# Performance work log

Hardware: AMD Instinct MI355X
Metric: run time of the kernel (lower is better)

The kernel has to match this reference:

```python
import jax, jax.numpy as jnp
import numpy as np

B, S, H = 64, 4096, 512

def setup_inputs() -> dict:
    key = jax.random.key(0)
    ks = jax.random.split(key, 8)
    decoder_output = jax.random.normal(ks[0], (B, H), dtype=jnp.float32)
    encoder_output = jax.random.normal(ks[1], (B, S, 2 * H), dtype=jnp.float32)
    mask = jax.random.randint(ks[2], (B, S), 0, 2).astype(bool)
    mask = mask.at[:, 0].set(True)  # guarantee at least one valid position per row
    sc_h = 1.0 / np.sqrt(2 * H)
    sc_s = 1.0 / np.sqrt(H)
    W_h_w = jax.random.uniform(ks[3], (H, 2 * H), jnp.float32, -sc_h, sc_h)
    W_h_b = jax.random.uniform(ks[4], (H,), jnp.float32, -sc_h, sc_h)
    W_s_w = jax.random.uniform(ks[5], (H, H), jnp.float32, -sc_s, sc_s)
    W_s_b = jax.random.uniform(ks[6], (H,), jnp.float32, -sc_s, sc_s)
    v_w = jax.random.uniform(ks[7], (1, H), jnp.float32, -sc_s, sc_s)
    return {"decoder_output": decoder_output, "encoder_output": encoder_output,
            "mask": mask, "W_h_w": W_h_w, "W_h_b": W_h_b,
            "W_s_w": W_s_w, "W_s_b": W_s_b, "v_w": v_w}

def reference(decoder_output, encoder_output, mask, W_h_w, W_h_b, W_s_w, W_s_b, v_w):
    # enc proj: [B,S,H]; dec proj: [B,H] broadcast over S
    enc = jnp.einsum('bse,he->bsh', encoder_output, W_h_w) + W_h_b
    dec = decoder_output @ W_s_w.T + W_s_b  # [B,H]
    x = jnp.tanh(enc + dec[:, None, :])     # [B,S,H]
    scores = jnp.einsum('bsh,h->bs', x, v_w[0])  # [B,S]
    masked = jnp.where(mask, scores, -jnp.inf)
    return jax.nn.softmax(masked, axis=-1)
```

## Files before the change

### kernel.cpp

```cpp
#include <hip/hip_runtime.h>
#include <math.h>

typedef __attribute__((ext_vector_type(8))) short bf16x8;
typedef __attribute__((ext_vector_type(4))) float f32x4;
typedef __attribute__((ext_vector_type(4))) unsigned short u16x4;

#define NB 64
#define NS 4096
#define NH 512
#define NE 1024
#define APITCH 80

__device__ __forceinline__ unsigned short f2bf(float f) {
  unsigned int u = __float_as_uint(f);
  u += 0x7fffu + ((u >> 16) & 1u);
  return (unsigned short)(u >> 16);
}

__device__ __forceinline__ float fast_tanh(float x) {
  float e = __expf(2.0f * x);
  return 1.0f - 2.0f * __builtin_amdgcn_rcpf(e + 1.0f);
}

__global__ __launch_bounds__(256) void prep_b_kernel(const float* __restrict__ W,
                                                     unsigned short* __restrict__ Bp) {
  const int t = blockIdx.x * 256 + threadIdx.x;
  const int lane = t & 63;
  const int ni = (t >> 6) & 3;
  const int kb = (t >> 8) & 31;
  const int w = t >> 13;
  const int col = w * 64 + ni * 16 + (lane & 15);
  const int k0 = kb * 32 + (lane >> 4) * 8;
  const float* src = W + col * NE + k0;
  float4 a = *(const float4*)src;
  float4 b = *(const float4*)(src + 4);
  union { bf16x8 v; unsigned short u[8]; } p;
  p.u[0] = f2bf(a.x); p.u[1] = f2bf(a.y); p.u[2] = f2bf(a.z); p.u[3] = f2bf(a.w);
  p.u[4] = f2bf(b.x); p.u[5] = f2bf(b.y); p.u[6] = f2bf(b.z); p.u[7] = f2bf(b.w);
  *(bf16x8*)(Bp + (long long)t * 8) = p.v;
}

__global__ __launch_bounds__(512) void prep_dec_kernel(const float* __restrict__ dec,
                                                       const float* __restrict__ Wsw,
                                                       const float* __restrict__ Wsb,
                                                       const float* __restrict__ Whb,
                                                       float* __restrict__ decb) {
  int b = blockIdx.x;
  int h = threadIdx.x;
  const float4* dr = (const float4*)(dec + b * NH);
  const float4* wr = (const float4*)(Wsw + h * NH);
  float sum = Wsb[h] + Whb[h];
#pragma unroll 8
  for (int i = 0; i < NH / 4; ++i) {
    float4 a = dr[i], w = wr[i];
    sum += a.x * w.x + a.y * w.y + a.z * w.z + a.w * w.w;
  }
  decb[b * NH + h] = sum;
}

__global__ __launch_bounds__(512, 4) void fused_main(const float* __restrict__ enc,
                                                     const unsigned short* __restrict__ Bp,
                                                     const float* __restrict__ decb,
                                                     const float* __restrict__ vw,
                                                     float* __restrict__ scores) {
  __shared__ __align__(16) char As[2][64 * APITCH];
  __shared__ float ssc[64];

  const int tid = threadIdx.x;
  const int lane = tid & 63;
  const int wave = tid >> 6;
  const int r15 = lane & 15;
  const int c4 = lane >> 4;
  const long long m0 = (long long)blockIdx.x * 64;

  if (tid < 64) ssc[tid] = 0.0f;

  const int arow = tid >> 3;
  const int achk = tid & 7;
  const float* aload = enc + (m0 + arow) * NE + achk * 4;
  const int awr = arow * APITCH + achk * 8;
  const int rdb = r15 * APITCH + c4 * 16;

  const unsigned short* const bb = Bp + (long long)wave * 32 * 2048 + lane * 8;

  f32x4 acc[4][4];
#pragma unroll
  for (int mi = 0; mi < 4; ++mi)
#pragma unroll
    for (int ni = 0; ni < 4; ++ni) {
      f32x4 z = {0.f, 0.f, 0.f, 0.f};
      acc[mi][ni] = z;
    }

  bf16x8 bEv[4], bOd[4];
#pragma unroll
  for (int ni = 0; ni < 4; ++ni) bEv[ni] = *(const bf16x8*)(bb + ni * 512);
  {
    float4 a0 = *(const float4*)(aload);
    unsigned int w0, w1;
    asm("v_cvt_pk_bf16_f32 %0, %1, %2" : "=v"(w0) : "v"(a0.x), "v"(a0.y));
    asm("v_cvt_pk_bf16_f32 %0, %1, %2" : "=v"(w1) : "v"(a0.z), "v"(a0.w));
    uint2 wv; wv.x = w0; wv.y = w1;
    *(uint2*)(&As[0][0] + awr) = wv;
  }
  asm volatile("s_waitcnt lgkmcnt(0)" ::: "memory");
  __builtin_amdgcn_s_barrier();

#pragma unroll
  for (int t = 0; t < 32; ++t) {
    float4 aT;
    if (t < 31) {
      aT = *(const float4*)(aload + (t + 1) * 32);
      const bf16x8* bp = (const bf16x8*)(bb + (t + 1) * 2048);
      if (t & 1) {
#pragma unroll
        for (int ni = 0; ni < 4; ++ni) bEv[ni] = bp[ni * 64];
      } else {
#pragma unroll
        for (int ni = 0; ni < 4; ++ni) bOd[ni] = bp[ni * 64];
      }
    }
    const char* Ab = &As[t & 1][0];
    bf16x8 af0 = *(const bf16x8*)(Ab + rdb);
    bf16x8 af1 = *(const bf16x8*)(Ab + 16 * APITCH + rdb);
    bf16x8 af2 = *(const bf16x8*)(Ab + 32 * APITCH + rdb);
    bf16x8 af3 = *(const bf16x8*)(Ab + 48 * APITCH + rdb);
    __builtin_amdgcn_sched_barrier(0);
    __builtin_amdgcn_s_setprio(1);
#pragma unroll
    for (int ni = 0; ni < 4; ++ni)
      acc[0][ni] = __builtin_amdgcn_mfma_f32_16x16x32_bf16(
          af0, (t & 1) ? bOd[ni] : bEv[ni], acc[0][ni], 0, 0, 0);
#pragma unroll
    for (int ni = 0; ni < 4; ++ni)
      acc[1][ni] = __builtin_amdgcn_mfma_f32_16x16x32_bf16(
          af1, (t & 1) ? bOd[ni] : bEv[ni], acc[1][ni], 0, 0, 0);
#pragma unroll
    for (int ni = 0; ni < 4; ++ni)
      acc[2][ni] = __builtin_amdgcn_mfma_f32_16x16x32_bf16(
          af2, (t & 1) ? bOd[ni] : bEv[ni], acc[2][ni], 0, 0, 0);
#pragma unroll
    for (int ni = 0; ni < 4; ++ni)
      acc[3][ni] = __builtin_amdgcn_mfma_f32_16x16x32_bf16(
          af3, (t & 1) ? bOd[ni] : bEv[ni], acc[3][ni], 0, 0, 0);
    __builtin_amdgcn_s_setprio(0);
    if (t < 31) {
      unsigned int w0, w1;
      asm("v_cvt_pk_bf16_f32 %0, %1, %2" : "=v"(w0) : "v"(aT.x), "v"(aT.y));
      asm("v_cvt_pk_bf16_f32 %0, %1, %2" : "=v"(w1) : "v"(aT.z), "v"(aT.w));
      uint2 wv; wv.x = w0; wv.y = w1;
      *(uint2*)(&As[(t + 1) & 1][0] + awr) = wv;
    }
    asm volatile("s_waitcnt lgkmcnt(0)" ::: "memory");
    __builtin_amdgcn_sched_barrier(0);
    __builtin_amdgcn_s_barrier();
  }

  const int bidx = (int)(m0 >> 12);
  const float* decrow = decb + bidx * NH;
  float part[4][4];
#pragma unroll
  for (int mi = 0; mi < 4; ++mi)
#pragma unroll
    for (int j = 0; j < 4; ++j) part[mi][j] = 0.f;

#pragma unroll
  for (int ni = 0; ni < 4; ++ni) {
    int col = (wave << 6) + ni * 16 + r15;
    float vc = vw[col];
    float dc = decrow[col];
#pragma unroll
    for (int mi = 0; mi < 4; ++mi)
#pragma unroll
      for (int j = 0; j < 4; ++j)
        part[mi][j] += vc * fast_tanh(acc[mi][ni][j] + dc);
  }
#pragma unroll
  for (int off = 1; off < 16; off <<= 1)
#pragma unroll
    for (int mi = 0; mi < 4; ++mi)
#pragma unroll
      for (int j = 0; j < 4; ++j)
        part[mi][j] += __shfl_xor(part[mi][j], off, 64);

  if (r15 == 0) {
#pragma unroll
    for (int mi = 0; mi < 4; ++mi)
#pragma unroll
      for (int j = 0; j < 4; ++j)
        atomicAdd(&ssc[mi * 16 + c4 * 4 + j], part[mi][j]);
  }
  __syncthreads();
  if (tid < 64) scores[m0 + tid] = ssc[tid];
}

__global__ __launch_bounds__(1024) void softmax_kernel(const float* __restrict__ scores,
                                                       const int* __restrict__ mask,
                                                       float* __restrict__ out) {
  __shared__ float rmax[16];
  __shared__ float rsum[16];
  const int b = blockIdx.x;
  const int t = threadIdx.x;
  const int wid = t >> 6;
  const int ln = t & 63;
  const int base = b * NS;

  float s[4];
  int mk[4];
  float mx = -INFINITY;
#pragma unroll
  for (int i = 0; i < 4; ++i) {
    int idx = t + i * 1024;
    s[i] = scores[base + idx];
    mk[i] = mask[base + idx];
    if (mk[i]) mx = fmaxf(mx, s[i]);
  }
#pragma unroll
  for (int off = 1; off < 64; off <<= 1) mx = fmaxf(mx, __shfl_xor(mx, off, 64));
  if (ln == 0) rmax[wid] = mx;
  __syncthreads();
  float m2 = -INFINITY;
#pragma unroll
  for (int i = 0; i < 16; ++i) m2 = fmaxf(m2, rmax[i]);

  float e[4];
  float sum = 0.f;
#pragma unroll
  for (int i = 0; i < 4; ++i) {
    e[i] = mk[i] ? expf(s[i] - m2) : 0.f;
    sum += e[i];
  }
#pragma unroll
  for (int off = 1; off < 64; off <<= 1) sum += __shfl_xor(sum, off, 64);
  if (ln == 0) rsum[wid] = sum;
  __syncthreads();
  float tot = 0.f;
#pragma unroll
  for (int i = 0; i < 16; ++i) tot += rsum[i];
  float inv = 1.0f / tot;
#pragma unroll
  for (int i = 0; i < 4; ++i) {
    int idx = t + i * 1024;
    out[base + idx] = e[i] * inv;
  }
}

extern "C" void kernel_launch(void* const* d_in, const int* in_sizes, int n_in,
                              void* d_out, int out_size, void* d_ws, size_t ws_size,
                              hipStream_t stream) {
  const float* dec = (const float*)d_in[0];
  const float* enc = (const float*)d_in[1];
  const int* mask = (const int*)d_in[2];
  const float* Whw = (const float*)d_in[3];
  const float* Whb = (const float*)d_in[4];
  const float* Wsw = (const float*)d_in[5];
  const float* Wsb = (const float*)d_in[6];
  const float* vw = (const float*)d_in[7];
  float* out = (float*)d_out;

  unsigned short* Bp = (unsigned short*)d_ws;
  float* decb = (float*)((char*)d_ws + (1 << 20));
  float* scoresb = (float*)((char*)d_ws + (1 << 20) + (128 << 10));

  prep_b_kernel<<<dim3(256), dim3(256), 0, stream>>>(Whw, Bp);
  prep_dec_kernel<<<dim3(64), dim3(512), 0, stream>>>(dec, Wsw, Wsb, Whb, decb);
  fused_main<<<dim3(4096), dim3(512), 0, stream>>>(enc, Bp, decb, vw, scoresb);
  softmax_kernel<<<dim3(64), dim3(1024), 0, stream>>>(scoresb, mask, out);
}
```

Baseline: 435.7 us.

## Double M tile to 128 rows with 4-stage LDS ring and fragment prefetch

Each block now covers 128 encoder rows instead of 64, so every W_h fragment read from global memory feeds twice as many MFMAs, halving B-operand traffic per output. The A tile is staged through a 4-deep LDS ring with global loads issued two steps ahead, and A fragments for the next step are read from LDS between MFMAs. The cost is twice the accumulator registers and LDS per block, with occupancy lowered to 2 blocks per CU, which may reduce latency hiding.

```diff
diff --git a/kernel.cpp b/kernel.cpp
--- a/kernel.cpp
+++ b/kernel.cpp
@@ -58,34 +58,34 @@
   decb[b * NH + h] = sum;
 }
 
-__global__ __launch_bounds__(512, 4) void fused_main(const float* __restrict__ enc,
+__global__ __launch_bounds__(512, 2) void fused_main(const float* __restrict__ enc,
                                                      const unsigned short* __restrict__ Bp,
                                                      const float* __restrict__ decb,
                                                      const float* __restrict__ vw,
                                                      float* __restrict__ scores) {
-  __shared__ __align__(16) char As[2][64 * APITCH];
-  __shared__ float ssc[64];
+  __shared__ __align__(16) char As[4][128 * APITCH];
+  __shared__ float ssc[128];
 
   const int tid = threadIdx.x;
   const int lane = tid & 63;
   const int wave = tid >> 6;
   const int r15 = lane & 15;
   const int c4 = lane >> 4;
-  const long long m0 = (long long)blockIdx.x * 64;
-
-  if (tid < 64) ssc[tid] = 0.0f;
-
-  const int arow = tid >> 3;
-  const int achk = tid & 7;
-  const float* aload = enc + (m0 + arow) * NE + achk * 4;
-  const int awr = arow * APITCH + achk * 8;
+  const long long m0 = (long long)blockIdx.x * 128;
+
+  if (tid < 128) ssc[tid] = 0.0f;
+
+  const int arow = tid >> 2;
+  const int achk = tid & 3;
+  const float* aload = enc + (m0 + arow) * NE + achk * 8;
+  const int awr = arow * APITCH + achk * 16;
   const int rdb = r15 * APITCH + c4 * 16;
 
   const unsigned short* const bb = Bp + (long long)wave * 32 * 2048 + lane * 8;
 
-  f32x4 acc[4][4];
-#pragma unroll
-  for (int mi = 0; mi < 4; ++mi)
+  f32x4 acc[8][4];
+#pragma unroll
+  for (int mi = 0; mi < 8; ++mi)
 #pragma unroll
     for (int ni = 0; ni < 4; ++ni) {
       f32x4 z = {0.f, 0.f, 0.f, 0.f};
@@ -95,22 +95,30 @@
   bf16x8 bEv[4], bOd[4];
 #pragma unroll
   for (int ni = 0; ni < 4; ++ni) bEv[ni] = *(const bf16x8*)(bb + ni * 512);
-  {
-    float4 a0 = *(const float4*)(aload);
-    unsigned int w0, w1;
-    asm("v_cvt_pk_bf16_f32 %0, %1, %2" : "=v"(w0) : "v"(a0.x), "v"(a0.y));
-    asm("v_cvt_pk_bf16_f32 %0, %1, %2" : "=v"(w1) : "v"(a0.z), "v"(a0.w));
-    uint2 wv; wv.x = w0; wv.y = w1;
-    *(uint2*)(&As[0][0] + awr) = wv;
-  }
+#pragma unroll
+  for (int s = 0; s < 2; ++s) {
+    float4 p0 = *(const float4*)(aload + s * 32);
+    float4 p1 = *(const float4*)(aload + s * 32 + 4);
+    uint4 wv;
+    asm("v_cvt_pk_bf16_f32 %0, %1, %2" : "=v"(wv.x) : "v"(p0.x), "v"(p0.y));
+    asm("v_cvt_pk_bf16_f32 %0, %1, %2" : "=v"(wv.y) : "v"(p0.z), "v"(p0.w));
+    asm("v_cvt_pk_bf16_f32 %0, %1, %2" : "=v"(wv.z) : "v"(p1.x), "v"(p1.y));
+    asm("v_cvt_pk_bf16_f32 %0, %1, %2" : "=v"(wv.w) : "v"(p1.z), "v"(p1.w));
+    *(uint4*)(&As[s][0] + awr) = wv;
+  }
+  float4 ap0 = *(const float4*)(aload + 64);
+  float4 ap1 = *(const float4*)(aload + 64 + 4);
   asm volatile("s_waitcnt lgkmcnt(0)" ::: "memory");
   __builtin_amdgcn_s_barrier();
 
+  bf16x8 af[8];
+#pragma unroll
+  for (int mi = 0; mi < 8; ++mi)
+    af[mi] = *(const bf16x8*)(&As[0][0] + mi * 16 * APITCH + rdb);
+
 #pragma unroll
   for (int t = 0; t < 32; ++t) {
-    float4 aT;
     if (t < 31) {
-      aT = *(const float4*)(aload + (t + 1) * 32);
       const bf16x8* bp = (const bf16x8*)(bb + (t + 1) * 2048);
       if (t & 1) {
 #pragma unroll
@@ -120,36 +128,28 @@
         for (int ni = 0; ni < 4; ++ni) bOd[ni] = bp[ni * 64];
       }
     }
-    const char* Ab = &As[t & 1][0];
-    bf16x8 af0 = *(const bf16x8*)(Ab + rdb);
-    bf16x8 af1 = *(const bf16x8*)(Ab + 16 * APITCH + rdb);
-    bf16x8 af2 = *(const bf16x8*)(Ab + 32 * APITCH + rdb);
-    bf16x8 af3 = *(const bf16x8*)(Ab + 48 * APITCH + rdb);
-    __builtin_amdgcn_sched_barrier(0);
+    if (t < 30) {
+      ap0 = *(const float4*)(aload + (t + 2) * 32);
+      ap1 = *(const float4*)(aload + (t + 2) * 32 + 4);
+    }
+    const char* Abn = &As[(t + 1) & 3][0];
     __builtin_amdgcn_s_setprio(1);
 #pragma unroll
-    for (int ni = 0; ni < 4; ++ni)
-      acc[0][ni] = __builtin_amdgcn_mfma_f32_16x16x32_bf16(
-          af0, (t & 1) ? bOd[ni] : bEv[ni], acc[0][ni], 0, 0, 0);
-#pragma unroll
-    for (int ni = 0; ni < 4; ++ni)
-      acc[1][ni] = __builtin_amdgcn_mfma_f32_16x16x32_bf16(
-          af1, (t & 1) ? bOd[ni] : bEv[ni], acc[1][ni], 0, 0, 0);
-#pragma unroll
-    for (int ni = 0; ni < 4; ++ni)
-      acc[2][ni] = __builtin_amdgcn_mfma_f32_16x16x32_bf16(
-          af2, (t & 1) ? bOd[ni] : bEv[ni], acc[2][ni], 0, 0, 0);
-#pragma unroll
-    for (int ni = 0; ni < 4; ++ni)
-      acc[3][ni] = __builtin_amdgcn_mfma_f32_16x16x32_bf16(
-          af3, (t & 1) ? bOd[ni] : bEv[ni], acc[3][ni], 0, 0, 0);
+    for (int mi = 0; mi < 8; ++mi) {
+#pragma unroll
+      for (int ni = 0; ni < 4; ++ni)
+        acc[mi][ni] = __builtin_amdgcn_mfma_f32_16x16x32_bf16(
+            af[mi], (t & 1) ? bOd[ni] : bEv[ni], acc[mi][ni], 0, 0, 0);
+      if (t < 31) af[mi] = *(const bf16x8*)(Abn + mi * 16 * APITCH + rdb);
+    }
     __builtin_amdgcn_s_setprio(0);
-    if (t < 31) {
-      unsigned int w0, w1;
-      asm("v_cvt_pk_bf16_f32 %0, %1, %2" : "=v"(w0) : "v"(aT.x), "v"(aT.y));
-      asm("v_cvt_pk_bf16_f32 %0, %1, %2" : "=v"(w1) : "v"(aT.z), "v"(aT.w));
-      uint2 wv; wv.x = w0; wv.y = w1;
-      *(uint2*)(&As[(t + 1) & 1][0] + awr) = wv;
+    if (t < 30) {
+      uint4 wv;
+      asm("v_cvt_pk_bf16_f32 %0, %1, %2" : "=v"(wv.x) : "v"(ap0.x), "v"(ap0.y));
+      asm("v_cvt_pk_bf16_f32 %0, %1, %2" : "=v"(wv.y) : "v"(ap0.z), "v"(ap0.w));
+      asm("v_cvt_pk_bf16_f32 %0, %1, %2" : "=v"(wv.z) : "v"(ap1.x), "v"(ap1.y));
+      asm("v_cvt_pk_bf16_f32 %0, %1, %2" : "=v"(wv.w) : "v"(ap1.z), "v"(ap1.w));
+      *(uint4*)(&As[(t + 2) & 3][0] + awr) = wv;
     }
     asm volatile("s_waitcnt lgkmcnt(0)" ::: "memory");
     __builtin_amdgcn_sched_barrier(0);
@@ -158,9 +158,9 @@
 
   const int bidx = (int)(m0 >> 12);
   const float* decrow = decb + bidx * NH;
-  float part[4][4];
-#pragma unroll
-  for (int mi = 0; mi < 4; ++mi)
+  float part[8][4];
+#pragma unroll
+  for (int mi = 0; mi < 8; ++mi)
 #pragma unroll
     for (int j = 0; j < 4; ++j) part[mi][j] = 0.f;
 
@@ -170,7 +170,7 @@
     float vc = vw[col];
     float dc = decrow[col];
 #pragma unroll
-    for (int mi = 0; mi < 4; ++mi)
+    for (int mi = 0; mi < 8; ++mi)
 #pragma unroll
       for (int j = 0; j < 4; ++j)
         part[mi][j] += vc * fast_tanh(acc[mi][ni][j] + dc);
@@ -178,20 +178,20 @@
 #pragma unroll
   for (int off = 1; off < 16; off <<= 1)
 #pragma unroll
-    for (int mi = 0; mi < 4; ++mi)
+    for (int mi = 0; mi < 8; ++mi)
 #pragma unroll
       for (int j = 0; j < 4; ++j)
         part[mi][j] += __shfl_xor(part[mi][j], off, 64);
 
   if (r15 == 0) {
 #pragma unroll
-    for (int mi = 0; mi < 4; ++mi)
+    for (int mi = 0; mi < 8; ++mi)
 #pragma unroll
       for (int j = 0; j < 4; ++j)
         atomicAdd(&ssc[mi * 16 + c4 * 4 + j], part[mi][j]);
   }
   __syncthreads();
-  if (tid < 64) scores[m0 + tid] = ssc[tid];
+  if (tid < 128) scores[m0 + tid] = ssc[tid];
 }
 
 __global__ __launch_bounds__(1024) void softmax_kernel(const float* __restrict__ scores,
@@ -264,6 +264,6 @@
 
   prep_b_kernel<<<dim3(256), dim3(256), 0, stream>>>(Whw, Bp);
   prep_dec_kernel<<<dim3(64), dim3(512), 0, stream>>>(dec, Wsw, Wsb, Whb, decb);
-  fused_main<<<dim3(4096), dim3(512), 0, stream>>>(enc, Bp, decb, vw, scoresb);
+  fused_main<<<dim3(2048), dim3(512), 0, stream>>>(enc, Bp, decb, vw, scoresb);
   softmax_kernel<<<dim3(64), dim3(1024), 0, stream>>>(scoresb, mask, out);
 }
```

After: 449.2 us. +3.1%, slower.

## Use 1024-thread blocks with 128-row tiles and deeper A prefetch

Applied to the files above, without the earlier changes.

The main GEMM kernel now processes 128 rows per block with 16 waves arranged as 2 row groups by 8 column groups. Each B fragment loaded from the weight buffer is therefore shared across twice as many rows, and the block count is halved. The encoder loads are now software-pipelined three steps ahead using rotating registers, to hide more global latency. The B double buffer is replaced by a single buffer loaded after the MFMAs, and the sched_barrier is removed. This raises register pressure and block size, which may reduce occupancy or expose B load latency.

```diff
diff --git a/kernel.cpp b/kernel.cpp
--- a/kernel.cpp
+++ b/kernel.cpp
@@ -28,8 +28,8 @@
   const int lane = t & 63;
   const int ni = (t >> 6) & 3;
   const int kb = (t >> 8) & 31;
-  const int w = t >> 13;
-  const int col = w * 64 + ni * 16 + (lane & 15);
+  const int g = t >> 13;
+  const int col = g * 64 + ni * 16 + (lane & 15);
   const int k0 = kb * 32 + (lane >> 4) * 8;
   const float* src = W + col * NE + k0;
   float4 a = *(const float4*)src;
@@ -58,30 +58,32 @@
   decb[b * NH + h] = sum;
 }
 
-__global__ __launch_bounds__(512, 4) void fused_main(const float* __restrict__ enc,
-                                                     const unsigned short* __restrict__ Bp,
-                                                     const float* __restrict__ decb,
-                                                     const float* __restrict__ vw,
-                                                     float* __restrict__ scores) {
-  __shared__ __align__(16) char As[2][64 * APITCH];
-  __shared__ float ssc[64];
+__global__ __launch_bounds__(1024, 4) void fused_main(const float* __restrict__ enc,
+                                                      const unsigned short* __restrict__ Bp,
+                                                      const float* __restrict__ decb,
+                                                      const float* __restrict__ vw,
+                                                      float* __restrict__ scores) {
+  __shared__ __align__(16) char As[2][128 * APITCH];
+  __shared__ float ssc[128];
 
   const int tid = threadIdx.x;
   const int lane = tid & 63;
   const int wave = tid >> 6;
+  const int wn = wave & 7;
+  const int wm = wave >> 3;
   const int r15 = lane & 15;
   const int c4 = lane >> 4;
-  const long long m0 = (long long)blockIdx.x * 64;
-
-  if (tid < 64) ssc[tid] = 0.0f;
+  const long long m0 = (long long)blockIdx.x * 128;
+
+  if (tid < 128) ssc[tid] = 0.0f;
 
   const int arow = tid >> 3;
-  const int achk = tid & 7;
-  const float* aload = enc + (m0 + arow) * NE + achk * 4;
-  const int awr = arow * APITCH + achk * 8;
-  const int rdb = r15 * APITCH + c4 * 16;
-
-  const unsigned short* const bb = Bp + (long long)wave * 32 * 2048 + lane * 8;
+  const int agk = tid & 7;
+  const float* aload = enc + (m0 + arow) * NE + agk * 4;
+  const int awr = arow * APITCH + agk * 8;
+  const int rdb = (wm * 64 + r15) * APITCH + c4 * 16;
+
+  const unsigned short* const bb = Bp + (long long)wn * 32 * 2048 + lane * 8;
 
   f32x4 acc[4][4];
 #pragma unroll
@@ -92,9 +94,9 @@
       acc[mi][ni] = z;
     }
 
-  bf16x8 bEv[4], bOd[4];
-#pragma unroll
-  for (int ni = 0; ni < 4; ++ni) bEv[ni] = *(const bf16x8*)(bb + ni * 512);
+  bf16x8 bcur[4];
+#pragma unroll
+  for (int ni = 0; ni < 4; ++ni) bcur[ni] = *(const bf16x8*)(bb + ni * 512);
   {
     float4 a0 = *(const float4*)(aload);
     unsigned int w0, w1;
@@ -103,51 +105,52 @@
     uint2 wv; wv.x = w0; wv.y = w1;
     *(uint2*)(&As[0][0] + awr) = wv;
   }
+  float4 s0, s1, s2;
+  s1 = *(const float4*)(aload + 1 * 32);
+  s2 = *(const float4*)(aload + 2 * 32);
   asm volatile("s_waitcnt lgkmcnt(0)" ::: "memory");
   __builtin_amdgcn_s_barrier();
 
 #pragma unroll
   for (int t = 0; t < 32; ++t) {
-    float4 aT;
-    if (t < 31) {
-      aT = *(const float4*)(aload + (t + 1) * 32);
-      const bf16x8* bp = (const bf16x8*)(bb + (t + 1) * 2048);
-      if (t & 1) {
-#pragma unroll
-        for (int ni = 0; ni < 4; ++ni) bEv[ni] = bp[ni * 64];
-      } else {
-#pragma unroll
-        for (int ni = 0; ni < 4; ++ni) bOd[ni] = bp[ni * 64];
-      }
+    if (t < 29) {
+      const float4* ap = (const float4*)(aload + (t + 3) * 32);
+      if (t % 3 == 0)      s0 = *ap;
+      else if (t % 3 == 1) s1 = *ap;
+      else                 s2 = *ap;
     }
     const char* Ab = &As[t & 1][0];
     bf16x8 af0 = *(const bf16x8*)(Ab + rdb);
     bf16x8 af1 = *(const bf16x8*)(Ab + 16 * APITCH + rdb);
     bf16x8 af2 = *(const bf16x8*)(Ab + 32 * APITCH + rdb);
     bf16x8 af3 = *(const bf16x8*)(Ab + 48 * APITCH + rdb);
-    __builtin_amdgcn_sched_barrier(0);
     __builtin_amdgcn_s_setprio(1);
 #pragma unroll
     for (int ni = 0; ni < 4; ++ni)
-      acc[0][ni] = __builtin_amdgcn_mfma_f32_16x16x32_bf16(
-          af0, (t & 1) ? bOd[ni] : bEv[ni], acc[0][ni], 0, 0, 0);
-#pragma unroll
-    for (int ni = 0; ni < 4; ++ni)
-      acc[1][ni] = __builtin_amdgcn_mfma_f32_16x16x32_bf16(
-          af1, (t & 1) ? bOd[ni] : bEv[ni], acc[1][ni], 0, 0, 0);
-#pragma unroll
-    for (int ni = 0; ni < 4; ++ni)
-      acc[2][ni] = __builtin_amdgcn_mfma_f32_16x16x32_bf16(
-          af2, (t & 1) ? bOd[ni] : bEv[ni], acc[2][ni], 0, 0, 0);
-#pragma unroll
-    for (int ni = 0; ni < 4; ++ni)
-      acc[3][ni] = __builtin_amdgcn_mfma_f32_16x16x32_bf16(
-          af3, (t & 1) ? bOd[ni] : bEv[ni], acc[3][ni], 0, 0, 0);
+      acc[0][ni] = __builtin_amdgcn_mfma_f32_16x16x32_bf16(af0, bcur[ni], acc[0][ni], 0, 0, 0);
+#pragma unroll
+    for (int ni = 0; ni < 4; ++ni)
+      acc[1][ni] = __builtin_amdgcn_mfma_f32_16x16x32_bf16(af1, bcur[ni], acc[1][ni], 0, 0, 0);
+#pragma unroll
+    for (int ni = 0; ni < 4; ++ni)
+      acc[2][ni] = __builtin_amdgcn_mfma_f32_16x16x32_bf16(af2, bcur[ni], acc[2][ni], 0, 0, 0);
+#pragma unroll
+    for (int ni = 0; ni < 4; ++ni)
+      acc[3][ni] = __builtin_amdgcn_mfma_f32_16x16x32_bf16(af3, bcur[ni], acc[3][ni], 0, 0, 0);
     __builtin_amdgcn_s_setprio(0);
     if (t < 31) {
+      const bf16x8* bp = (const bf16x8*)(bb + (t + 1) * 2048);
+#pragma unroll
+      for (int ni = 0; ni < 4; ++ni) bcur[ni] = bp[ni * 64];
+    }
+    if (t < 31) {
+      float4 a;
+      if (t % 3 == 0)      a = s1;
+      else if (t % 3 == 1) a = s2;
+      else                 a = s0;
       unsigned int w0, w1;
-      asm("v_cvt_pk_bf16_f32 %0, %1, %2" : "=v"(w0) : "v"(aT.x), "v"(aT.y));
-      asm("v_cvt_pk_bf16_f32 %0, %1, %2" : "=v"(w1) : "v"(aT.z), "v"(aT.w));
+      asm("v_cvt_pk_bf16_f32 %0, %1, %2" : "=v"(w0) : "v"(a.x), "v"(a.y));
+      asm("v_cvt_pk_bf16_f32 %0, %1, %2" : "=v"(w1) : "v"(a.z), "v"(a.w));
       uint2 wv; wv.x = w0; wv.y = w1;
       *(uint2*)(&As[(t + 1) & 1][0] + awr) = wv;
     }
@@ -166,7 +169,7 @@
 
 #pragma unroll
   for (int ni = 0; ni < 4; ++ni) {
-    int col = (wave << 6) + ni * 16 + r15;
+    int col = (wn << 6) + ni * 16 + r15;
     float vc = vw[col];
     float dc = decrow[col];
 #pragma unroll
@@ -188,10 +191,10 @@
     for (int mi = 0; mi < 4; ++mi)
 #pragma unroll
       for (int j = 0; j < 4; ++j)
-        atomicAdd(&ssc[mi * 16 + c4 * 4 + j], part[mi][j]);
+        atomicAdd(&ssc[wm * 64 + mi * 16 + c4 * 4 + j], part[mi][j]);
   }
   __syncthreads();
-  if (tid < 64) scores[m0 + tid] = ssc[tid];
+  if (tid < 128) scores[m0 + tid] = ssc[tid];
 }
 
 __global__ __launch_bounds__(1024) void softmax_kernel(const float* __restrict__ scores,
@@ -264,6 +267,6 @@
 
   prep_b_kernel<<<dim3(256), dim3(256), 0, stream>>>(Whw, Bp);
   prep_dec_kernel<<<dim3(64), dim3(512), 0, stream>>>(dec, Wsw, Wsb, Whb, decb);
-  fused_main<<<dim3(4096), dim3(512), 0, stream>>>(enc, Bp, decb, vw, scoresb);
+  fused_main<<<dim3(2048), dim3(1024), 0, stream>>>(enc, Bp, decb, vw, scoresb);
   softmax_kernel<<<dim3(64), dim3(1024), 0, stream>>>(scoresb, mask, out);
 }
```

New measurement: 400.3 us. -8.1%, faster.

## Load A fragments directly from global per wave, dropping LDS staging and barriers

Applied to the files above, without the earlier changes.

Each wave now reads its encoder A fragments straight from global memory into registers and converts them to bf16 in place, replacing the shared-memory double buffer and the per-iteration block barriers. The intent is to remove LDS traffic and synchronisation stalls from the K loop. The cost is that all 8 waves redundantly fetch the same 64x1024 fp32 A tile (8x more global/L2 reads), with strided per-lane access and load latency exposed one fragment ahead.

```diff
diff --git a/kernel.cpp b/kernel.cpp
--- a/kernel.cpp
+++ b/kernel.cpp
@@ -9,7 +9,6 @@
 #define NS 4096
 #define NH 512
 #define NE 1024
-#define APITCH 80
 
 __device__ __forceinline__ unsigned short f2bf(float f) {
   unsigned int u = __float_as_uint(f);
@@ -28,8 +27,8 @@
   const int lane = t & 63;
   const int ni = (t >> 6) & 3;
   const int kb = (t >> 8) & 31;
-  const int w = t >> 13;
-  const int col = w * 64 + ni * 16 + (lane & 15);
+  const int g = t >> 13;
+  const int col = g * 64 + ni * 16 + (lane & 15);
   const int k0 = kb * 32 + (lane >> 4) * 8;
   const float* src = W + col * NE + k0;
   float4 a = *(const float4*)src;
@@ -63,7 +62,6 @@
                                                      const float* __restrict__ decb,
                                                      const float* __restrict__ vw,
                                                      float* __restrict__ scores) {
-  __shared__ __align__(16) char As[2][64 * APITCH];
   __shared__ float ssc[64];
 
   const int tid = threadIdx.x;
@@ -75,11 +73,10 @@
 
   if (tid < 64) ssc[tid] = 0.0f;
 
-  const int arow = tid >> 3;
-  const int achk = tid & 7;
-  const float* aload = enc + (m0 + arow) * NE + achk * 4;
-  const int awr = arow * APITCH + achk * 8;
-  const int rdb = r15 * APITCH + c4 * 16;
+  const float* ab0 = enc + (m0 + 0 * 16 + r15) * NE + c4 * 8;
+  const float* ab1 = enc + (m0 + 1 * 16 + r15) * NE + c4 * 8;
+  const float* ab2 = enc + (m0 + 2 * 16 + r15) * NE + c4 * 8;
+  const float* ab3 = enc + (m0 + 3 * 16 + r15) * NE + c4 * 8;
 
   const unsigned short* const bb = Bp + (long long)wave * 32 * 2048 + lane * 8;
 
@@ -95,66 +92,50 @@
   bf16x8 bEv[4], bOd[4];
 #pragma unroll
   for (int ni = 0; ni < 4; ++ni) bEv[ni] = *(const bf16x8*)(bb + ni * 512);
-  {
-    float4 a0 = *(const float4*)(aload);
-    unsigned int w0, w1;
-    asm("v_cvt_pk_bf16_f32 %0, %1, %2" : "=v"(w0) : "v"(a0.x), "v"(a0.y));
-    asm("v_cvt_pk_bf16_f32 %0, %1, %2" : "=v"(w1) : "v"(a0.z), "v"(a0.w));
-    uint2 wv; wv.x = w0; wv.y = w1;
-    *(uint2*)(&As[0][0] + awr) = wv;
-  }
-  asm volatile("s_waitcnt lgkmcnt(0)" ::: "memory");
-  __builtin_amdgcn_s_barrier();
+  f32x4 a0 = *(const f32x4*)(ab0);
+  f32x4 a1 = *(const f32x4*)(ab0 + 4);
 
 #pragma unroll
   for (int t = 0; t < 32; ++t) {
-    float4 aT;
-    if (t < 31) {
-      aT = *(const float4*)(aload + (t + 1) * 32);
-      const bf16x8* bp = (const bf16x8*)(bb + (t + 1) * 2048);
-      if (t & 1) {
-#pragma unroll
-        for (int ni = 0; ni < 4; ++ni) bEv[ni] = bp[ni * 64];
-      } else {
-#pragma unroll
-        for (int ni = 0; ni < 4; ++ni) bOd[ni] = bp[ni * 64];
+#pragma unroll
+    for (int mi = 0; mi < 4; ++mi) {
+      bf16x8 af;
+      {
+        union { unsigned int u[4]; bf16x8 v; } pk;
+        asm("v_cvt_pk_bf16_f32 %0, %1, %2" : "=v"(pk.u[0]) : "v"(a0.x), "v"(a0.y));
+        asm("v_cvt_pk_bf16_f32 %0, %1, %2" : "=v"(pk.u[1]) : "v"(a0.z), "v"(a0.w));
+        asm("v_cvt_pk_bf16_f32 %0, %1, %2" : "=v"(pk.u[2]) : "v"(a1.x), "v"(a1.y));
+        asm("v_cvt_pk_bf16_f32 %0, %1, %2" : "=v"(pk.u[3]) : "v"(a1.z), "v"(a1.w));
+        af = pk.v;
       }
+      const int ng = t * 4 + mi + 1;
+      if (ng < 128) {
+        const int tn = ng >> 2;
+        const int mn = ng & 3;
+        const float* p = (mn == 0 ? ab0 : mn == 1 ? ab1 : mn == 2 ? ab2 : ab3) + tn * 32;
+        a0 = *(const f32x4*)p;
+        a1 = *(const f32x4*)(p + 4);
+      }
+      if (mi == 0 && t < 31) {
+        const bf16x8* bp = (const bf16x8*)(bb + (t + 1) * 2048);
+        if (t & 1) {
+#pragma unroll
+          for (int ni = 0; ni < 4; ++ni) bEv[ni] = bp[ni * 64];
+        } else {
+#pragma unroll
+          for (int ni = 0; ni < 4; ++ni) bOd[ni] = bp[ni * 64];
+        }
+      }
+      __builtin_amdgcn_s_setprio(1);
+#pragma unroll
+      for (int ni = 0; ni < 4; ++ni)
+        acc[mi][ni] = __builtin_amdgcn_mfma_f32_16x16x32_bf16(
+            af, (t & 1) ? bOd[ni] : bEv[ni], acc[mi][ni], 0, 0, 0);
+      __builtin_amdgcn_s_setprio(0);
     }
-    const char* Ab = &As[t & 1][0];
-    bf16x8 af0 = *(const bf16x8*)(Ab + rdb);
-    bf16x8 af1 = *(const bf16x8*)(Ab + 16 * APITCH + rdb);
-    bf16x8 af2 = *(const bf16x8*)(Ab + 32 * APITCH + rdb);
-    bf16x8 af3 = *(const bf16x8*)(Ab + 48 * APITCH + rdb);
-    __builtin_amdgcn_sched_barrier(0);
-    __builtin_amdgcn_s_setprio(1);
-#pragma unroll
-    for (int ni = 0; ni < 4; ++ni)
-      acc[0][ni] = __builtin_amdgcn_mfma_f32_16x16x32_bf16(
-          af0, (t & 1) ? bOd[ni] : bEv[ni], acc[0][ni], 0, 0, 0);
-#pragma unroll
-    for (int ni = 0; ni < 4; ++ni)
-      acc[1][ni] = __builtin_amdgcn_mfma_f32_16x16x32_bf16(
-          af1, (t & 1) ? bOd[ni] : bEv[ni], acc[1][ni], 0, 0, 0);
-#pragma unroll
-    for (int ni = 0; ni < 4; ++ni)
-      acc[2][ni] = __builtin_amdgcn_mfma_f32_16x16x32_bf16(
-          af2, (t & 1) ? bOd[ni] : bEv[ni], acc[2][ni], 0, 0, 0);
-#pragma unroll
-    for (int ni = 0; ni < 4; ++ni)
-      acc[3][ni] = __builtin_amdgcn_mfma_f32_16x16x32_bf16(
-          af3, (t & 1) ? bOd[ni] : bEv[ni], acc[3][ni], 0, 0, 0);
-    __builtin_amdgcn_s_setprio(0);
-    if (t < 31) {
-      unsigned int w0, w1;
-      asm("v_cvt_pk_bf16_f32 %0, %1, %2" : "=v"(w0) : "v"(aT.x), "v"(aT.y));
-      asm("v_cvt_pk_bf16_f32 %0, %1, %2" : "=v"(w1) : "v"(aT.z), "v"(aT.w));
-      uint2 wv; wv.x = w0; wv.y = w1;
-      *(uint2*)(&As[(t + 1) & 1][0] + awr) = wv;
-    }
-    asm volatile("s_waitcnt lgkmcnt(0)" ::: "memory");
-    __builtin_amdgcn_sched_barrier(0);
-    __builtin_amdgcn_s_barrier();
-  }
+  }
+
+  __syncthreads();
 
   const int bidx = (int)(m0 >> 12);
   const float* decrow = decb + bidx * NH;
```

New measurement: 1.161 ms. 2.66x slower.
